# Performance work log

Measured on AMD Instinct MI355X. Metric: run time of the kernel, lower is better.

Reference implementation:

```python
import jax, jax.numpy as jnp
import numpy as np

N = 100000
E = 3200000
D = 128
EPS = 1e-12  # F.normalize default eps


def setup_inputs() -> dict:
    key = jax.random.key(0)
    ks = jax.random.split(key, 8)
    inp = {
        "edge_index": jax.random.randint(ks[0], (2, E), 0, N, dtype=jnp.int64)
        if jax.config.jax_enable_x64 else jax.random.randint(ks[0], (2, E), 0, N, dtype=jnp.int32),
        "emb_weight": jax.random.normal(ks[1], (N, D), dtype=jnp.float32) / np.sqrt(D),
        "lin_l_w0": jax.random.normal(ks[2], (D, D), dtype=jnp.float32) / np.sqrt(D),
        "lin_l_b0": jax.random.normal(ks[3], (D,), dtype=jnp.float32) * 0.01,
        "lin_r_w0": jax.random.normal(ks[4], (D, D), dtype=jnp.float32) / np.sqrt(D),
        "lin_l_w1": jax.random.normal(ks[5], (D, D), dtype=jnp.float32) / np.sqrt(D),
        "lin_l_b1": jax.random.normal(ks[6], (D,), dtype=jnp.float32) * 0.01,
        "lin_r_w1": jax.random.normal(ks[7], (D, D), dtype=jnp.float32) / np.sqrt(D),
    }
    return inp


def _sage_conv(x, src, dst, deg_inv, lin_l_w, lin_l_b, lin_r_w):
    # mean aggregation of source features at destination nodes
    agg = jax.ops.segment_sum(x[src], dst, num_segments=N) * deg_inv  # [N, D]
    # out = lin_l(agg) + lin_r(x); torch Linear: y = x @ W.T + b
    return agg @ lin_l_w.T + lin_l_b + x @ lin_r_w.T


def reference(edge_index, emb_weight, lin_l_w0, lin_l_b0, lin_r_w0,
              lin_l_w1, lin_l_b1, lin_r_w1):
    src, dst = edge_index[0], edge_index[1]
    deg = jax.ops.segment_sum(jnp.ones((E,), jnp.float32), dst, num_segments=N)
    deg_inv = jnp.where(deg > 0, 1.0 / jnp.maximum(deg, 1.0), 0.0)[:, None]  # [N,1]

    x = emb_weight
    x = _sage_conv(x, src, dst, deg_inv, lin_l_w0, lin_l_b0, lin_r_w0)
    x = jax.nn.relu(x)
    x = _sage_conv(x, src, dst, deg_inv, lin_l_w1, lin_l_b1, lin_r_w1)
    # F.normalize(x, p=2, dim=1): x / max(||x||_2, eps)
    norm = jnp.linalg.norm(x, axis=1, keepdims=True)
    return x / jnp.maximum(norm, EPS)
```

## Files before the change

kernel.cpp:

```cpp
#include <hip/hip_runtime.h>

typedef unsigned int uint;
typedef unsigned short ushort;
typedef __bf16 v8b __attribute__((ext_vector_type(8)));
typedef float v4f __attribute__((ext_vector_type(4)));

#define NN 100000
#define EE 3200000
#define DD 128

#define BSH 8
#define BSZ 256
#define NB ((NN + BSZ - 1) / BSZ)
#define CAP 16384
#define EPB 8192
#define NBLK1 ((EE + EPB - 1) / EPB)

#define LGRID ((NN + 127) / 128)

#define PREP_EMB 12500
#define PREP_WB 16
#define PREP_BIAS (PREP_EMB + 4 * PREP_WB)
#define PREP_ZERO (PREP_BIAS + 1)
#define PREP_GRID (PREP_ZERO + 2)

__device__ __attribute__((aligned(256))) int g_offs[NN + 1];
__device__ __attribute__((aligned(256))) int g_flag[2];
__device__ __attribute__((aligned(256))) int g_bcnt2[NB];
__device__ __attribute__((aligned(256))) int g_bbase[NB];
__device__ __attribute__((aligned(256))) int g_csr[EE];
__device__ __attribute__((aligned(256))) uint g_pairs2[(size_t)NB * CAP];
__device__ __attribute__((aligned(256))) ushort g_emb_h[(size_t)NN * DD];
__device__ __attribute__((aligned(256))) ushort g_emb_l[(size_t)NN * DD];
__device__ __attribute__((aligned(256))) ushort g_agg_h[(size_t)NN * DD];
__device__ __attribute__((aligned(256))) ushort g_agg_l[(size_t)NN * DD];
__device__ __attribute__((aligned(256))) ushort g_hh[(size_t)NN * DD];
__device__ __attribute__((aligned(256))) ushort g_hl[(size_t)NN * DD];
__device__ __attribute__((aligned(256))) ushort g_w_h[4][DD * DD];
__device__ __attribute__((aligned(256))) ushort g_w_l[4][DD * DD];
__device__ __attribute__((aligned(256))) float g_biasf[2][DD];

__device__ __forceinline__ float blo(uint u) { return __uint_as_float(u << 16); }
__device__ __forceinline__ float bhi(uint u) { return __uint_as_float(u & 0xffff0000u); }
__device__ __forceinline__ ushort f2b(float f) {
  uint u = __float_as_uint(f);
  u += 0x7fffu + ((u >> 16) & 1u);
  return (ushort)(u >> 16);
}
__device__ __forceinline__ float b2f(ushort s) { return __uint_as_float(((uint)s) << 16); }

__global__ void k_detect_ei(const int* __restrict__ ei) {
  __shared__ int any;
  if (threadIdx.x == 0) any = 0;
  __syncthreads();
  int v = 0;
  for (int i = threadIdx.x; i < 2048; i += 256) v |= ei[2 * i + 1];
  if (v) atomicOr(&any, 1);
  __syncthreads();
  if (threadIdx.x == 0) g_flag[0] = (any == 0) ? 1 : 0;
}

__global__ void k_detect_f(const ushort* __restrict__ u) {
  __shared__ int bad;
  if (threadIdx.x == 0) bad = 0;
  __syncthreads();
  int b = 0;
  for (int i = threadIdx.x; i < 2048; i += 256) {
    int e = (u[2 * i] >> 7) & 0xff;
    if (e < 0x40 || e > 0x7f) b = 1;
  }
  if (b) atomicOr(&bad, 1);
  __syncthreads();
  if (threadIdx.x == 0) g_flag[1] = bad;
}

__device__ __forceinline__ void split4(const void* __restrict__ src,
                                       ushort* __restrict__ dh,
                                       ushort* __restrict__ dl, int i) {
  float f[4];
  if (g_flag[1]) {
    float4 v = *(const float4*)((const float*)src + i);
    f[0] = v.x; f[1] = v.y; f[2] = v.z; f[3] = v.w;
  } else {
    ushort4 s = *(const ushort4*)((const ushort*)src + i);
    f[0] = b2f(s.x); f[1] = b2f(s.y); f[2] = b2f(s.z); f[3] = b2f(s.w);
  }
  ushort4 h, l;
  ushort* hp = &h.x;
  ushort* lp = &l.x;
#pragma unroll
  for (int k = 0; k < 4; k++) {
    ushort hi = f2b(f[k]);
    hp[k] = hi;
    lp[k] = f2b(f[k] - b2f(hi));
  }
  *(ushort4*)(dh + i) = h;
  *(ushort4*)(dl + i) = l;
}

__global__ void k_prep(const void* __restrict__ emb, const void* __restrict__ s0,
                       const void* __restrict__ s1, const void* __restrict__ s2,
                       const void* __restrict__ s3, const void* __restrict__ bs0,
                       const void* __restrict__ bs1) {
  int bid = blockIdx.x;
  int tid = threadIdx.x;
  if (bid < PREP_EMB) {
    int i = (bid * 256 + tid) * 4;
    split4(emb, g_emb_h, g_emb_l, i);
  } else if (bid < PREP_BIAS) {
    int wb = bid - PREP_EMB;
    int w = wb >> 4;
    int i = ((wb & 15) * 256 + tid) * 4;
    const void* src = (w == 0) ? s0 : (w == 1) ? s1 : (w == 2) ? s2 : s3;
    split4(src, &g_w_h[0][0] + w * DD * DD, &g_w_l[0][0] + w * DD * DD, i);
  } else if (bid == PREP_BIAS) {
    int which = tid >> 7;
    int i = tid & 127;
    const void* src = which ? bs1 : bs0;
    float v = g_flag[1] ? ((const float*)src)[i] : b2f(((const ushort*)src)[i]);
    g_biasf[which][i] = v;
  } else {
    int i = (bid - PREP_ZERO) * 256 + tid;
    if (i < NB) g_bcnt2[i] = 0;
  }
}

__device__ __forceinline__ int ld_src(const int* __restrict__ ei, int is64, int e) {
  int v = is64 ? ei[2 * e] : ei[e];
  return ((uint)v < (uint)NN) ? v : 0;
}
__device__ __forceinline__ int ld_dst(const int* __restrict__ ei, int is64, int e) {
  int v = is64 ? ei[2 * (EE + e)] : ei[EE + e];
  return ((uint)v < (uint)NN) ? v : 0;
}


__global__ __launch_bounds__(256) void k_bucket(const int* __restrict__ ei) {
  int is64 = g_flag[0];
  __shared__ uint s_pk[EPB];
  __shared__ ushort s_bk[EPB];
  __shared__ int s_cnt[NB];
  __shared__ int s_base[NB];
  for (int i = threadIdx.x; i < NB; i += 256) s_cnt[i] = 0;
  __syncthreads();
  int base = blockIdx.x * EPB;
#pragma unroll
  for (int i = 0; i < EPB / 256; i++) {
    int li = i * 256 + threadIdx.x;
    int e = base + li;
    uint pk = 0;
    int b = -1;
    if (e < EE) {
      int d = ld_dst(ei, is64, e);
      int s = ld_src(ei, is64, e);
      b = d >> BSH;
      pk = ((uint)(d & (BSZ - 1)) << 17) | (uint)s;
      atomicAdd(&s_cnt[b], 1);
    }
    s_pk[li] = pk;
    s_bk[li] = (ushort)b;
  }
  __syncthreads();
  for (int i = threadIdx.x; i < NB; i += 256) {
    int c = s_cnt[i];
    s_base[i] = c ? atomicAdd(&g_bcnt2[i], c) : 0;
    s_cnt[i] = 0;
  }
  __syncthreads();
#pragma unroll
  for (int i = 0; i < EPB / 256; i++) {
    int li = i * 256 + threadIdx.x;
    int b = s_bk[li];
    if (b != 0xffff) {
      int idx = s_base[b] + atomicAdd(&s_cnt[b], 1);
      if (idx < CAP) g_pairs2[(size_t)b * CAP + idx] = s_pk[li];
    }
  }
}

__global__ void k_bscan() {
  __shared__ int sd[512];
  int t = threadIdx.x;
  int v = (t < NB) ? min(g_bcnt2[t], CAP) : 0;
  sd[t] = v;
  __syncthreads();
  for (int off = 1; off < 512; off <<= 1) {
    int x = (t >= off) ? sd[t - off] : 0;
    __syncthreads();
    sd[t] += x;
    __syncthreads();
  }
  if (t < NB) g_bbase[t] = sd[t] - v;
  if (t == 511) g_offs[NN] = sd[511];
}

__global__ __launch_bounds__(256) void k_place() {
  int b = blockIdx.x;
  int n = min(g_bcnt2[b], CAP);
  int gbase = g_bbase[b];
  const uint* pr = g_pairs2 + (size_t)b * CAP;
  __shared__ int hist[BSZ];
  __shared__ int sd[BSZ];
  __shared__ int cur[BSZ];
  int t = threadIdx.x;
  hist[t] = 0;
  __syncthreads();
  for (int e = t; e < n; e += 256) atomicAdd(&hist[pr[e] >> 17], 1);
  __syncthreads();
  int v = hist[t];
  sd[t] = v;
  __syncthreads();
  for (int off = 1; off < BSZ; off <<= 1) {
    int x = (t >= off) ? sd[t - off] : 0;
    __syncthreads();
    sd[t] += x;
    __syncthreads();
  }
  int excl = sd[t] - v;
  int node = (b << BSH) + t;
  if (node < NN) g_offs[node] = gbase + excl;
  cur[t] = excl;
  __syncthreads();
  for (int e = t; e < n; e += 256) {
    uint pk = pr[e];
    int p = atomicAdd(&cur[pk >> 17], 1);
    g_csr[gbase + p] = (int)(pk & 0x1FFFFu);
  }
}

__global__ void k_agg(const ushort* __restrict__ x) {
  int lane = threadIdx.x & 63;
  int node = (blockIdx.x * blockDim.x + threadIdx.x) >> 6;
  int beg = g_offs[node], end = g_offs[node + 1];
  int eb = lane >> 4;
  int col = (lane & 15) * 8;
  float a[8];
#pragma unroll
  for (int i = 0; i < 8; i++) a[i] = 0.f;
  for (int c = beg; c < end; c += 64) {
    int cnt = end - c;
    if (cnt > 64) cnt = 64;
    int my = g_csr[c + (lane < cnt ? lane : cnt - 1)];
    if ((uint)my >= (uint)NN) my = 0;
    int j = 0;
    for (; j + 8 <= cnt; j += 8) {
      int s0 = __shfl(my, j + eb);
      int s1 = __shfl(my, j + 4 + eb);
      uint4 r0 = *(const uint4*)(x + (size_t)s0 * DD + col);
      uint4 r1 = *(const uint4*)(x + (size_t)s1 * DD + col);
      a[0] += blo(r0.x); a[1] += bhi(r0.x);
      a[2] += blo(r0.y); a[3] += bhi(r0.y);
      a[4] += blo(r0.z); a[5] += bhi(r0.z);
      a[6] += blo(r0.w); a[7] += bhi(r0.w);
      a[0] += blo(r1.x); a[1] += bhi(r1.x);
      a[2] += blo(r1.y); a[3] += bhi(r1.y);
      a[4] += blo(r1.z); a[5] += bhi(r1.z);
      a[6] += blo(r1.w); a[7] += bhi(r1.w);
    }
    for (; j < cnt; j += 4) {
      int e = j + eb;
      int s = __shfl(my, e < cnt ? e : 0);
      float w = e < cnt ? 1.f : 0.f;
      uint4 r = *(const uint4*)(x + (size_t)s * DD + col);
      a[0] = fmaf(blo(r.x), w, a[0]); a[1] = fmaf(bhi(r.x), w, a[1]);
      a[2] = fmaf(blo(r.y), w, a[2]); a[3] = fmaf(bhi(r.y), w, a[3]);
      a[4] = fmaf(blo(r.z), w, a[4]); a[5] = fmaf(bhi(r.z), w, a[5]);
      a[6] = fmaf(blo(r.w), w, a[6]); a[7] = fmaf(bhi(r.w), w, a[7]);
    }
  }
#pragma unroll
  for (int i = 0; i < 8; i++) {
    a[i] += __shfl_xor(a[i], 16);
    a[i] += __shfl_xor(a[i], 32);
  }
  int deg = end - beg;
  float inv = deg > 0 ? 1.0f / (float)deg : 0.f;
  if (lane < 16) {
    uint4 h, l;
    uint* hp = &h.x;
    uint* lp = &l.x;
#pragma unroll
    for (int k = 0; k < 4; k++) {
      float f0 = a[2 * k] * inv, f1 = a[2 * k + 1] * inv;
      ushort h0 = f2b(f0), h1 = f2b(f1);
      ushort l0 = f2b(f0 - b2f(h0)), l1 = f2b(f1 - b2f(h1));
      hp[k] = (uint)h0 | ((uint)h1 << 16);
      lp[k] = (uint)l0 | ((uint)l1 << 16);
    }
    size_t o = (size_t)node * DD + col;
    *(uint4*)(g_agg_h + o) = h;
    *(uint4*)(g_agg_l + o) = l;
  }
}


#define MFMA16(a, b, c) __builtin_amdgcn_mfma_f32_16x16x32_bf16(a, b, c, 0, 0, 0)

template <int MODE>
__global__ __launch_bounds__(256, 2) void k_lin(
    const ushort* __restrict__ A1h, const ushort* __restrict__ A1l,
    const ushort* __restrict__ A2h, const ushort* __restrict__ A2l,
    const ushort* __restrict__ Wlh, const ushort* __restrict__ Wll,
    const ushort* __restrict__ Wrh, const ushort* __restrict__ Wrl,
    const float* __restrict__ bias, void* out0, ushort* __restrict__ outlo) {
  __shared__ ushort smem[16384];
  int tid = threadIdx.x;
  int lane = tid & 63;
  int wid = tid >> 6;
  int m = lane & 15, q = lane >> 4;
  int row0 = blockIdx.x * 128 + wid * 32;
  int arow0 = row0 + m;      if (arow0 > NN - 1) arow0 = NN - 1;
  int arow1 = row0 + 16 + m; if (arow1 > NN - 1) arow1 = NN - 1;
  size_t aoff0 = (size_t)arow0 * DD + q * 8;
  size_t aoff1 = (size_t)arow1 * DD + q * 8;
  v8b a1h[2][4], a1l[2][4], a2h[2][4], a2l[2][4];
#pragma unroll
  for (int ks = 0; ks < 4; ks++) {
    a1h[0][ks] = *(const v8b*)(A1h + aoff0 + ks * 32);
    a1l[0][ks] = *(const v8b*)(A1l + aoff0 + ks * 32);
    a2h[0][ks] = *(const v8b*)(A2h + aoff0 + ks * 32);
    a2l[0][ks] = *(const v8b*)(A2l + aoff0 + ks * 32);
    a1h[1][ks] = *(const v8b*)(A1h + aoff1 + ks * 32);
    a1l[1][ks] = *(const v8b*)(A1l + aoff1 + ks * 32);
    a2h[1][ks] = *(const v8b*)(A2h + aoff1 + ks * 32);
    a2l[1][ks] = *(const v8b*)(A2l + aoff1 + ks * 32);
  }
  v4f acc[2][8];
#pragma unroll
  for (int t = 0; t < 2; t++)
#pragma unroll
    for (int nt = 0; nt < 8; nt++) acc[t][nt] = (v4f){0.f, 0.f, 0.f, 0.f};
#pragma unroll
  for (int st = 0; st < 4; st++) {
#pragma unroll
    for (int k = 0; k < 8; k++) {
      int arr = k >> 1;
      int n = ((k & 1) << 4) + (tid >> 4);
      int cb16 = tid & 15;
      const ushort* srcp = (arr == 0) ? Wlh : (arr == 1) ? Wll : (arr == 2) ? Wrh : Wrl;
      uint4 v = *(const uint4*)(srcp + (size_t)(st * 32 + n) * DD + cb16 * 8);
      *(uint4*)(smem + arr * 4096 + n * 128 + ((cb16 ^ (n & 15)) << 3)) = v;
    }
    __syncthreads();
#pragma unroll
    for (int ks = 0; ks < 4; ks++) {
#pragma unroll
      for (int ntl = 0; ntl < 2; ntl++) {
        int nt = st * 2 + ntl;
        int nl = ntl * 16 + m;
        int u = nl * 128 + (((q + 4 * ks) ^ m) << 3);
        v8b blh = *(const v8b*)(smem + u);
        v8b bll = *(const v8b*)(smem + 4096 + u);
        v8b brh = *(const v8b*)(smem + 8192 + u);
        v8b brl = *(const v8b*)(smem + 12288 + u);
        acc[0][nt] = MFMA16(a1h[0][ks], blh, acc[0][nt]);
        acc[0][nt] = MFMA16(a1h[0][ks], bll, acc[0][nt]);
        acc[0][nt] = MFMA16(a1l[0][ks], blh, acc[0][nt]);
        acc[0][nt] = MFMA16(a2h[0][ks], brh, acc[0][nt]);
        acc[0][nt] = MFMA16(a2h[0][ks], brl, acc[0][nt]);
        acc[0][nt] = MFMA16(a2l[0][ks], brh, acc[0][nt]);
        acc[1][nt] = MFMA16(a1h[1][ks], blh, acc[1][nt]);
        acc[1][nt] = MFMA16(a1h[1][ks], bll, acc[1][nt]);
        acc[1][nt] = MFMA16(a1l[1][ks], blh, acc[1][nt]);
        acc[1][nt] = MFMA16(a2h[1][ks], brh, acc[1][nt]);
        acc[1][nt] = MFMA16(a2h[1][ks], brl, acc[1][nt]);
        acc[1][nt] = MFMA16(a2l[1][ks], brh, acc[1][nt]);
      }
    }
    __syncthreads();
  }
  if (MODE == 0) {
    ushort* oh = (ushort*)out0;
#pragma unroll
    for (int t = 0; t < 2; t++) {
#pragma unroll
      for (int nt = 0; nt < 8; nt++) {
        float bv = bias[nt * 16 + m];
#pragma unroll
        for (int r = 0; r < 4; r++) {
          int row = row0 + t * 16 + q * 4 + r;
          if (row < NN) {
            float v = acc[t][nt][r] + bv;
            v = v > 0.f ? v : 0.f;
            ushort hi = f2b(v);
            ushort lo = f2b(v - b2f(hi));
            size_t o = (size_t)row * DD + nt * 16 + m;
            oh[o] = hi;
            outlo[o] = lo;
          }
        }
      }
    }
  } else {
    float* of = (float*)out0;
#pragma unroll
    for (int t = 0; t < 2; t++) {
#pragma unroll
      for (int r = 0; r < 4; r++) {
        float p = 0.f;
#pragma unroll
        for (int nt = 0; nt < 8; nt++) {
          float v = acc[t][nt][r] + bias[nt * 16 + m];
          acc[t][nt][r] = v;
          p += v * v;
        }
        p += __shfl_xor(p, 1);
        p += __shfl_xor(p, 2);
        p += __shfl_xor(p, 4);
        p += __shfl_xor(p, 8);
        float inv = (p > 0.f) ? 1.0f / fmaxf(sqrtf(p), 1e-12f) : 0.f;
        int row = row0 + t * 16 + q * 4 + r;
        if (row < NN) {
#pragma unroll
          for (int nt = 0; nt < 8; nt++)
            of[(size_t)row * DD + nt * 16 + m] = acc[t][nt][r] * inv;
        }
      }
    }
  }
}


extern "C" void kernel_launch(void* const* d_in, const int* in_sizes, int n_in,
                              void* d_out, int out_size, void* d_ws, size_t ws_size,
                              hipStream_t stream) {
  const int* ei = (const int*)d_in[0];
  (void)in_sizes; (void)n_in; (void)out_size; (void)d_ws; (void)ws_size;

  ushort* wh;  hipGetSymbolAddress((void**)&wh, HIP_SYMBOL(g_w_h));
  ushort* wl;  hipGetSymbolAddress((void**)&wl, HIP_SYMBOL(g_w_l));
  ushort* wl0h = wh, *wr0h = wh + DD * DD, *wl1h = wh + 2 * DD * DD, *wr1h = wh + 3 * DD * DD;
  ushort* wl0l = wl, *wr0l = wl + DD * DD, *wl1l = wl + 2 * DD * DD, *wr1l = wl + 3 * DD * DD;
  float* bf;   hipGetSymbolAddress((void**)&bf, HIP_SYMBOL(g_biasf));
  float* b0 = bf, *b1 = bf + DD;
  ushort* eh;  hipGetSymbolAddress((void**)&eh, HIP_SYMBOL(g_emb_h));
  ushort* el;  hipGetSymbolAddress((void**)&el, HIP_SYMBOL(g_emb_l));
  ushort* ah;  hipGetSymbolAddress((void**)&ah, HIP_SYMBOL(g_agg_h));
  ushort* al;  hipGetSymbolAddress((void**)&al, HIP_SYMBOL(g_agg_l));
  ushort* hh;  hipGetSymbolAddress((void**)&hh, HIP_SYMBOL(g_hh));
  ushort* hl;  hipGetSymbolAddress((void**)&hl, HIP_SYMBOL(g_hl));

  k_detect_ei<<<1, 256, 0, stream>>>(ei);
  k_detect_f<<<1, 256, 0, stream>>>((const ushort*)d_in[1]);

  k_prep<<<PREP_GRID, 256, 0, stream>>>(d_in[1], d_in[2], d_in[4], d_in[5],
                                        d_in[7], d_in[3], d_in[6]);

  k_bucket<<<NBLK1, 256, 0, stream>>>(ei);
  k_bscan<<<1, 512, 0, stream>>>();
  k_place<<<NB, 256, 0, stream>>>();

  k_agg<<<NN / 4, 256, 0, stream>>>(eh);
  k_lin<0><<<LGRID, 256, 0, stream>>>(ah, al, eh, el, wl0h, wl0l, wr0h, wr0l, b0, hh, hl);
  k_agg<<<NN / 4, 256, 0, stream>>>(hh);
  k_lin<1><<<LGRID, 256, 0, stream>>>(ah, al, hh, hl, wl1h, wl1l, wr1h, wr1l, b1, d_out, nullptr);
}
```

Before: 507.6 us.

## Fuse dtype detection, prep and bucketing into one kernel; unroll gather

Four kernels (index-width detection, float-format detection, weight/embedding prep and edge bucketing) are merged into one launch. Index and float format are now detected per block, and bucketing blocks keep edge packs in registers instead of staging them in shared memory. The bucket counters are zeroed at the end of k_place rather than in prep, and the aggregation gather loop is unrolled to 16 edges so more row loads are in flight at once. The aim is to cut launch and serialization overhead and raise memory-level parallelism. The cost is extra register pressure and repeated detection work in every block, and the counter reset depends on g_bcnt2 starting at zero on the first call.

Result: faster. 495.1 us (-2.5%).

```diff
diff --git a/kernel.cpp b/kernel.cpp
--- a/kernel.cpp
+++ b/kernel.cpp
@@ -18,14 +18,14 @@
 
 #define LGRID ((NN + 127) / 128)
 
-#define PREP_EMB 12500
-#define PREP_WB 16
-#define PREP_BIAS (PREP_EMB + 4 * PREP_WB)
-#define PREP_ZERO (PREP_BIAS + 1)
-#define PREP_GRID (PREP_ZERO + 2)
+#define PB_B0 NBLK1
+#define PB_EMBB 12500
+#define PB_B1 (PB_B0 + PB_EMBB)
+#define PB_WB 64
+#define PB_B2 (PB_B1 + PB_WB)
+#define PB_GRID (PB_B2 + 1)
 
 __device__ __attribute__((aligned(256))) int g_offs[NN + 1];
-__device__ __attribute__((aligned(256))) int g_flag[2];
 __device__ __attribute__((aligned(256))) int g_bcnt2[NB];
 __device__ __attribute__((aligned(256))) int g_bbase[NB];
 __device__ __attribute__((aligned(256))) int g_csr[EE];
@@ -49,36 +49,20 @@
 }
 __device__ __forceinline__ float b2f(ushort s) { return __uint_as_float(((uint)s) << 16); }
 
-__global__ void k_detect_ei(const int* __restrict__ ei) {
-  __shared__ int any;
-  if (threadIdx.x == 0) any = 0;
-  __syncthreads();
-  int v = 0;
-  for (int i = threadIdx.x; i < 2048; i += 256) v |= ei[2 * i + 1];
-  if (v) atomicOr(&any, 1);
-  __syncthreads();
-  if (threadIdx.x == 0) g_flag[0] = (any == 0) ? 1 : 0;
-}
-
-__global__ void k_detect_f(const ushort* __restrict__ u) {
-  __shared__ int bad;
-  if (threadIdx.x == 0) bad = 0;
-  __syncthreads();
-  int b = 0;
-  for (int i = threadIdx.x; i < 2048; i += 256) {
-    int e = (u[2 * i] >> 7) & 0xff;
-    if (e < 0x40 || e > 0x7f) b = 1;
-  }
-  if (b) atomicOr(&bad, 1);
-  __syncthreads();
-  if (threadIdx.x == 0) g_flag[1] = bad;
-}
-
-__device__ __forceinline__ void split4(const void* __restrict__ src,
-                                       ushort* __restrict__ dh,
-                                       ushort* __restrict__ dl, int i) {
+__device__ __forceinline__ int ld_src(const int* __restrict__ ei, int is64, int e) {
+  int v = is64 ? ei[2 * e] : ei[e];
+  return ((uint)v < (uint)NN) ? v : 0;
+}
+__device__ __forceinline__ int ld_dst(const int* __restrict__ ei, int is64, int e) {
+  int v = is64 ? ei[2 * (EE + e)] : ei[EE + e];
+  return ((uint)v < (uint)NN) ? v : 0;
+}
+
+__device__ __forceinline__ void split4f(const void* __restrict__ src,
+                                        ushort* __restrict__ dh,
+                                        ushort* __restrict__ dl, int i, int isf32) {
   float f[4];
-  if (g_flag[1]) {
+  if (isf32) {
     float4 v = *(const float4*)((const float*)src + i);
     f[0] = v.x; f[1] = v.y; f[2] = v.z; f[3] = v.w;
   } else {
@@ -98,82 +82,90 @@
   *(ushort4*)(dl + i) = l;
 }
 
-__global__ void k_prep(const void* __restrict__ emb, const void* __restrict__ s0,
-                       const void* __restrict__ s1, const void* __restrict__ s2,
-                       const void* __restrict__ s3, const void* __restrict__ bs0,
-                       const void* __restrict__ bs1) {
+__global__ __launch_bounds__(256) void k_pb(
+    const int* __restrict__ ei, const void* __restrict__ emb,
+    const void* __restrict__ s0, const void* __restrict__ s1,
+    const void* __restrict__ s2, const void* __restrict__ s3,
+    const void* __restrict__ bs0, const void* __restrict__ bs1) {
+  __shared__ int s_cnt[NB];
+  __shared__ int s_base[NB];
+  __shared__ int s_flag;
   int bid = blockIdx.x;
   int tid = threadIdx.x;
-  if (bid < PREP_EMB) {
-    int i = (bid * 256 + tid) * 4;
-    split4(emb, g_emb_h, g_emb_l, i);
-  } else if (bid < PREP_BIAS) {
-    int wb = bid - PREP_EMB;
-    int w = wb >> 4;
-    int i = ((wb & 15) * 256 + tid) * 4;
-    const void* src = (w == 0) ? s0 : (w == 1) ? s1 : (w == 2) ? s2 : s3;
-    split4(src, &g_w_h[0][0] + w * DD * DD, &g_w_l[0][0] + w * DD * DD, i);
-  } else if (bid == PREP_BIAS) {
-    int which = tid >> 7;
-    int i = tid & 127;
-    const void* src = which ? bs1 : bs0;
-    float v = g_flag[1] ? ((const float*)src)[i] : b2f(((const ushort*)src)[i]);
-    g_biasf[which][i] = v;
+  if (bid < PB_B0) {
+    if (tid == 0) s_flag = 0;
+    for (int i = tid; i < NB; i += 256) s_cnt[i] = 0;
+    __syncthreads();
+    int base = bid * EPB;
+    int v = 0;
+#pragma unroll
+    for (int k = 0; k < 8; k++) {
+      int e = base + k * 256 + tid;
+      if (e < EE) v |= ei[2 * e + 1];
+    }
+    if (v) atomicOr(&s_flag, 1);
+    __syncthreads();
+    int is64 = (s_flag == 0) ? 1 : 0;
+    uint pk[32];
+    uint bb[16];
+#pragma unroll
+    for (int k = 0; k < 32; k++) {
+      int e = base + k * 256 + tid;
+      uint b = 0xffffu;
+      uint p = 0;
+      if (e < EE) {
+        int d = ld_dst(ei, is64, e);
+        int s = ld_src(ei, is64, e);
+        b = (uint)(d >> BSH);
+        p = ((uint)(d & (BSZ - 1)) << 17) | (uint)s;
+        atomicAdd(&s_cnt[(int)b], 1);
+      }
+      pk[k] = p;
+      if ((k & 1) == 0) bb[k >> 1] = b;
+      else bb[k >> 1] |= b << 16;
+    }
+    __syncthreads();
+    for (int i = tid; i < NB; i += 256) {
+      int c = s_cnt[i];
+      s_base[i] = c ? atomicAdd(&g_bcnt2[i], c) : 0;
+      s_cnt[i] = 0;
+    }
+    __syncthreads();
+#pragma unroll
+    for (int k = 0; k < 32; k++) {
+      uint b = (bb[k >> 1] >> ((k & 1) * 16)) & 0xffffu;
+      if (b != 0xffffu) {
+        int idx = s_base[b] + atomicAdd(&s_cnt[b], 1);
+        if (idx < CAP) g_pairs2[(size_t)b * CAP + idx] = pk[k];
+      }
+    }
   } else {
-    int i = (bid - PREP_ZERO) * 256 + tid;
-    if (i < NB) g_bcnt2[i] = 0;
-  }
-}
-
-__device__ __forceinline__ int ld_src(const int* __restrict__ ei, int is64, int e) {
-  int v = is64 ? ei[2 * e] : ei[e];
-  return ((uint)v < (uint)NN) ? v : 0;
-}
-__device__ __forceinline__ int ld_dst(const int* __restrict__ ei, int is64, int e) {
-  int v = is64 ? ei[2 * (EE + e)] : ei[EE + e];
-  return ((uint)v < (uint)NN) ? v : 0;
-}
-
-
-__global__ __launch_bounds__(256) void k_bucket(const int* __restrict__ ei) {
-  int is64 = g_flag[0];
-  __shared__ uint s_pk[EPB];
-  __shared__ ushort s_bk[EPB];
-  __shared__ int s_cnt[NB];
-  __shared__ int s_base[NB];
-  for (int i = threadIdx.x; i < NB; i += 256) s_cnt[i] = 0;
-  __syncthreads();
-  int base = blockIdx.x * EPB;
-#pragma unroll
-  for (int i = 0; i < EPB / 256; i++) {
-    int li = i * 256 + threadIdx.x;
-    int e = base + li;
-    uint pk = 0;
-    int b = -1;
-    if (e < EE) {
-      int d = ld_dst(ei, is64, e);
-      int s = ld_src(ei, is64, e);
-      b = d >> BSH;
-      pk = ((uint)(d & (BSZ - 1)) << 17) | (uint)s;
-      atomicAdd(&s_cnt[b], 1);
-    }
-    s_pk[li] = pk;
-    s_bk[li] = (ushort)b;
-  }
-  __syncthreads();
-  for (int i = threadIdx.x; i < NB; i += 256) {
-    int c = s_cnt[i];
-    s_base[i] = c ? atomicAdd(&g_bcnt2[i], c) : 0;
-    s_cnt[i] = 0;
-  }
-  __syncthreads();
-#pragma unroll
-  for (int i = 0; i < EPB / 256; i++) {
-    int li = i * 256 + threadIdx.x;
-    int b = s_bk[li];
-    if (b != 0xffff) {
-      int idx = s_base[b] + atomicAdd(&s_cnt[b], 1);
-      if (idx < CAP) g_pairs2[(size_t)b * CAP + idx] = s_pk[li];
+    if (tid == 0) s_flag = 0;
+    __syncthreads();
+    const ushort* u = (const ushort*)emb;
+    int bad = 0;
+    for (int i = tid; i < 2048; i += 256) {
+      int e = (u[2 * i] >> 7) & 0xff;
+      if (e < 0x40 || e > 0x7f) bad = 1;
+    }
+    if (bad) atomicOr(&s_flag, 1);
+    __syncthreads();
+    int isf32 = s_flag;
+    if (bid < PB_B1) {
+      int i = ((bid - PB_B0) * 256 + tid) * 4;
+      split4f(emb, g_emb_h, g_emb_l, i, isf32);
+    } else if (bid < PB_B2) {
+      int wb = bid - PB_B1;
+      int w = wb >> 4;
+      int i = ((wb & 15) * 256 + tid) * 4;
+      const void* src = (w == 0) ? s0 : (w == 1) ? s1 : (w == 2) ? s2 : s3;
+      split4f(src, &g_w_h[0][0] + w * DD * DD, &g_w_l[0][0] + w * DD * DD, i, isf32);
+    } else {
+      int which = tid >> 7;
+      int i = tid & 127;
+      const void* src = which ? bs1 : bs0;
+      float vv = isf32 ? ((const float*)src)[i] : b2f(((const ushort*)src)[i]);
+      g_biasf[which][i] = vv;
     }
   }
 }
@@ -226,6 +218,8 @@
     int p = atomicAdd(&cur[pk >> 17], 1);
     g_csr[gbase + p] = (int)(pk & 0x1FFFFu);
   }
+  __syncthreads();
+  if (t == 0) g_bcnt2[b] = 0;
 }
 
 __global__ void k_agg(const ushort* __restrict__ x) {
@@ -243,19 +237,33 @@
     int my = g_csr[c + (lane < cnt ? lane : cnt - 1)];
     if ((uint)my >= (uint)NN) my = 0;
     int j = 0;
+    for (; j + 16 <= cnt; j += 16) {
+      int s0 = __shfl(my, j + eb);
+      int s1 = __shfl(my, j + 4 + eb);
+      int s2 = __shfl(my, j + 8 + eb);
+      int s3 = __shfl(my, j + 12 + eb);
+      uint4 r0 = *(const uint4*)(x + (size_t)s0 * DD + col);
+      uint4 r1 = *(const uint4*)(x + (size_t)s1 * DD + col);
+      uint4 r2 = *(const uint4*)(x + (size_t)s2 * DD + col);
+      uint4 r3 = *(const uint4*)(x + (size_t)s3 * DD + col);
+      a[0] += blo(r0.x); a[1] += bhi(r0.x); a[2] += blo(r0.y); a[3] += bhi(r0.y);
+      a[4] += blo(r0.z); a[5] += bhi(r0.z); a[6] += blo(r0.w); a[7] += bhi(r0.w);
+      a[0] += blo(r1.x); a[1] += bhi(r1.x); a[2] += blo(r1.y); a[3] += bhi(r1.y);
+      a[4] += blo(r1.z); a[5] += bhi(r1.z); a[6] += blo(r1.w); a[7] += bhi(r1.w);
+      a[0] += blo(r2.x); a[1] += bhi(r2.x); a[2] += blo(r2.y); a[3] += bhi(r2.y);
+      a[4] += blo(r2.z); a[5] += bhi(r2.z); a[6] += blo(r2.w); a[7] += bhi(r2.w);
+      a[0] += blo(r3.x); a[1] += bhi(r3.x); a[2] += blo(r3.y); a[3] += bhi(r3.y);
+      a[4] += blo(r3.z); a[5] += bhi(r3.z); a[6] += blo(r3.w); a[7] += bhi(r3.w);
+    }
     for (; j + 8 <= cnt; j += 8) {
       int s0 = __shfl(my, j + eb);
       int s1 = __shfl(my, j + 4 + eb);
       uint4 r0 = *(const uint4*)(x + (size_t)s0 * DD + col);
       uint4 r1 = *(const uint4*)(x + (size_t)s1 * DD + col);
-      a[0] += blo(r0.x); a[1] += bhi(r0.x);
-      a[2] += blo(r0.y); a[3] += bhi(r0.y);
-      a[4] += blo(r0.z); a[5] += bhi(r0.z);
-      a[6] += blo(r0.w); a[7] += bhi(r0.w);
-      a[0] += blo(r1.x); a[1] += bhi(r1.x);
-      a[2] += blo(r1.y); a[3] += bhi(r1.y);
-      a[4] += blo(r1.z); a[5] += bhi(r1.z);
-      a[6] += blo(r1.w); a[7] += bhi(r1.w);
+      a[0] += blo(r0.x); a[1] += bhi(r0.x); a[2] += blo(r0.y); a[3] += bhi(r0.y);
+      a[4] += blo(r0.z); a[5] += bhi(r0.z); a[6] += blo(r0.w); a[7] += bhi(r0.w);
+      a[0] += blo(r1.x); a[1] += bhi(r1.x); a[2] += blo(r1.y); a[3] += bhi(r1.y);
+      a[4] += blo(r1.z); a[5] += bhi(r1.z); a[6] += blo(r1.w); a[7] += bhi(r1.w);
     }
     for (; j < cnt; j += 4) {
       int e = j + eb;
@@ -440,13 +448,8 @@
   ushort* hh;  hipGetSymbolAddress((void**)&hh, HIP_SYMBOL(g_hh));
   ushort* hl;  hipGetSymbolAddress((void**)&hl, HIP_SYMBOL(g_hl));
 
-  k_detect_ei<<<1, 256, 0, stream>>>(ei);
-  k_detect_f<<<1, 256, 0, stream>>>((const ushort*)d_in[1]);
-
-  k_prep<<<PREP_GRID, 256, 0, stream>>>(d_in[1], d_in[2], d_in[4], d_in[5],
-                                        d_in[7], d_in[3], d_in[6]);
-
-  k_bucket<<<NBLK1, 256, 0, stream>>>(ei);
+  k_pb<<<PB_GRID, 256, 0, stream>>>(ei, d_in[1], d_in[2], d_in[4], d_in[5],
+                                    d_in[7], d_in[3], d_in[6]);
   k_bscan<<<1, 512, 0, stream>>>();
   k_place<<<NB, 256, 0, stream>>>();
 
```
